# Performance work log

Hardware: AMD Instinct MI355X
Metric: run time of the kernel (lower is better)

The kernel has to match this reference:

```python
import jax, jax.numpy as jnp
import numpy as np
from jax import lax

B, N, CIN, COUT = 8, 4096, 64, 128
S, NS, V = 1024, 32, 4
RADIUS = 0.2
H1, H2 = 64, 128
BN_EPS = 1e-5


def _fps(xyz, n_sample):
    # farthest point sampling, deterministic start at index 0
    Bb, Nn, _ = xyz.shape
    start = jnp.zeros((Bb,), jnp.int32)
    mind0 = jnp.full((Bb, Nn), jnp.inf, xyz.dtype)

    def body(carry, _):
        mind, last = carry
        p = jnp.take_along_axis(xyz, last[:, None, None], axis=1)  # [B,1,3]
        d = jnp.sum((xyz - p) ** 2, -1)                             # [B,N]
        mind = jnp.minimum(mind, d)
        nxt = jnp.argmax(mind, -1).astype(jnp.int32)
        return (mind, nxt), nxt

    (_, _), rest = lax.scan(body, (mind0, start), None, length=n_sample - 1)
    idx = jnp.concatenate([start[None], rest], 0).T                 # [B,S]
    new_xyz = jnp.take_along_axis(xyz, idx[..., None], axis=1)      # [B,S,3]
    return new_xyz, idx


def _ball_query_idx(new_xyz, xyz, K, radius):
    # first K points (in index order) within radius, padded with -1
    d2 = jnp.sum((new_xyz[:, :, None, :] - xyz[:, None, :, :]) ** 2, -1)  # [B,S,N]
    within = d2 < radius * radius
    Nn = xyz.shape[1]
    ar = jnp.arange(Nn)
    key = jnp.where(within, ar, Nn + ar)            # in-ball points sort first, stably by index
    sel = jnp.argsort(key, axis=-1)[:, :, :K]       # [B,S,K]
    valid = jnp.take_along_axis(within, sel, axis=-1)
    return jnp.where(valid, sel, -1)


def _masked_gather(f, idx):
    # gather rows of f [B,N,C] with idx (any batched shape); idx==-1 -> zeros
    mask = idx == -1
    safe = jnp.where(mask, 0, idx)
    g = jax.vmap(lambda fb, ib: fb[ib])(f, safe)
    return jnp.where(mask[..., None], jnp.zeros((), f.dtype), g)


def _bn(x, gamma, beta, axes):
    # training-mode batchnorm over `axes` (channel is last dim)
    mu = jnp.mean(x, axes, keepdims=True)
    var = jnp.mean((x - mu) ** 2, axes, keepdims=True)
    return (x - mu) * (gamma / jnp.sqrt(var + BN_EPS)) + beta


def setup_inputs() -> dict:
    key = jax.random.key(0)
    ks = jax.random.split(key, 16)
    sc = 0.05
    inp = {
        "xyz": jax.random.uniform(ks[0], (B, N, 3), jnp.float32),
        "f": jax.random.normal(ks[1], (B, N, CIN), jnp.float32),
        "centroid_idx": jax.random.randint(ks[2], (V,), 0, NS),
        "affine_weight": jnp.ones((CIN + 6,), jnp.float32),
        "affine_bias": jnp.zeros((CIN + 6,), jnp.float32),
        "mix_w": sc * jax.random.normal(ks[3], (CIN, 2 * CIN + 6), jnp.float32),
        "mix_b": jnp.zeros((CIN,), jnp.float32),
        "m1_w1": sc * jax.random.normal(ks[4], (H1, 13), jnp.float32),
        "m1_b1": jnp.zeros((H1,), jnp.float32),
        "m1_g1": jnp.ones((H1,), jnp.float32),
        "m1_be1": jnp.zeros((H1,), jnp.float32),
        "m1_w2": sc * jax.random.normal(ks[5], (CIN, H1), jnp.float32),
        "m1_b2": jnp.zeros((CIN,), jnp.float32),
        "m2_w1": sc * jax.random.normal(ks[6], (H2, CIN), jnp.float32),
        "m2_b1": jnp.zeros((H2,), jnp.float32),
        "m2_g1": jnp.ones((H2,), jnp.float32),
        "m2_be1": jnp.zeros((H2,), jnp.float32),
        "m2_w2": sc * jax.random.normal(ks[7], (COUT, H2), jnp.float32),
        "m2_b2": jnp.zeros((COUT,), jnp.float32),
        "res_w": sc * jax.random.normal(ks[8], (COUT, CIN), jnp.float32),
        "res_b": jnp.zeros((COUT,), jnp.float32),
    }
    return inp


def reference(xyz, f, centroid_idx, affine_weight, affine_bias, mix_w, mix_b,
              m1_w1, m1_b1, m1_g1, m1_be1, m1_w2, m1_b2,
              m2_w1, m2_b1, m2_g1, m2_be1, m2_w2, m2_b2, res_w, res_b):
    Bb = xyz.shape[0]
    # ---- Grouping ----
    new_xyz, new_idx = _fps(xyz, S)                     # [B,S,3], [B,S]
    gidx = _ball_query_idx(new_xyz, xyz, NS, RADIUS)    # [B,S,n]
    mask = gidx == -1
    grouped_xyz = _masked_gather(xyz, gidx)             # [B,S,n,3]
    grouped_feat = _masked_gather(f, gidx)              # [B,S,n,cin]
    sampled = _masked_gather(f, new_idx)[:, :, None, :]  # [B,S,1,cin]
    gxl = grouped_xyz - new_xyz[:, :, None, :]
    gfl = grouped_feat - sampled
    gf = jnp.concatenate([grouped_xyz, gxl, gfl], -1)   # [B,S,n,cin+6]
    std = jnp.std(gf.reshape(Bb, -1), axis=-1, ddof=1).reshape(Bb, 1, 1, 1)
    gf = gf / (std + 1e-5)
    gf = affine_weight * gf + affine_bias
    gf = jnp.concatenate([gf, jnp.broadcast_to(sampled, (Bb, S, NS, CIN))], -1)
    grouped_f = jnp.einsum('bsnc,oc->bsno', gf, mix_w) + mix_b  # [B,S,n,cin]
    group_skip = grouped_f

    # ---- multi-centroid relative geometry (rel_jk, 13 channels) ----
    mc = xyz[:, centroid_idx, :]                                       # [B,V,3]
    arrow = grouped_xyz[:, :, :, None, :] - mc[:, None, None, :, :]    # [B,S,n,V,3]
    eu = jnp.sqrt(jnp.sum(arrow ** 2, -1, keepdims=True))              # [B,S,n,V,1]
    gx_b = jnp.broadcast_to(grouped_xyz[:, :, :, None, :], arrow.shape)
    mc_b = jnp.broadcast_to(mc[:, None, None, :, :], arrow.shape)
    rel = jnp.concatenate([-arrow, arrow, eu, gx_b, mc_b], -1)         # [B,S,n,V,13]

    # ---- m1: 1x1x1 Conv3d -> BN3d -> GELU -> Conv3d ----
    h = jnp.einsum('bsnvc,oc->bsnvo', rel, m1_w1) + m1_b1
    h = _bn(h, m1_g1, m1_be1, (0, 1, 2, 3))
    h = jax.nn.gelu(h, approximate=False)
    w_jk = jnp.einsum('bsnvc,oc->bsnvo', h, m1_w2) + m1_b2             # [B,S,n,V,cin]

    # ---- gumbel-softmax weighted aggregation over V centroids ----
    logits = grouped_f[:, :, :, None, :] * w_jk                        # [B,S,n,V,cin]
    u = jax.random.uniform(jax.random.key(42), logits.shape, logits.dtype, 1e-9, 1.0)
    gumbel = -jnp.log(-jnp.log(u))
    soft_w = jax.nn.softmax(logits + gumbel, axis=3)  # softmax over V (tau=1, soft)
    agg = jnp.sum(soft_w * logits, axis=3)                             # [B,S,n,cin]
    agg = agg + group_skip
    agg = jnp.where(mask[..., None], jnp.zeros((), agg.dtype), agg)

    # ---- m2: 1x1 Conv2d -> BN2d -> Conv2d, residual, max-pool over n ----
    h2 = jnp.einsum('bsnc,oc->bsno', agg, m2_w1) + m2_b1
    h2 = _bn(h2, m2_g1, m2_be1, (0, 1, 2))
    out = jnp.einsum('bsnc,oc->bsno', h2, m2_w2) + m2_b2               # [B,S,n,cout]
    res = jnp.einsum('bsnc,oc->bsno', group_skip, res_w) + res_b
    new_f = jax.nn.gelu(out + res, approximate=False)
    new_f = jnp.max(new_f, axis=2)                                     # [B,S,cout]
    return new_f, new_xyz
```

## Files before the change

kernel.cpp:

```cpp
#include <hip/hip_runtime.h>
#include <cstdint>
#include <cstddef>

#define TF_PARTITIONABLE 1

constexpr int B_ = 8, N_ = 4096, CIN_ = 64, COUT_ = 128;
constexpr int S_ = 1024, NS_ = 32, V_ = 4;
constexpr int ROWS_ = B_ * S_ * NS_;

constexpr size_t OFF_ACC   = 0;
constexpr size_t ACC_BYTES = 35072;
constexpr size_t OFF_SCALE = 35072;
constexpr size_t OFF_W1P   = 35328;
constexpr size_t OFF_B1P   = 38656;
constexpr size_t OFF_WCOMB = 38912;
constexpr size_t OFF_BCOMB = 71680;
constexpr size_t OFF_MIXWT = 72192;
constexpr size_t OFF_NIDX  = 106496;
constexpr size_t OFF_GIDX  = 139264;
constexpr size_t OFF_GF    = 1187840;
constexpr size_t OFF_AGG   = 68296704;

constexpr int AC_BATCH = 0;
constexpr int AC_G     = 16;
constexpr int AC_E     = 88;
constexpr int AC_S2A   = 216;
constexpr int AC_M2    = 280;

__device__ __forceinline__ float erf_fast(float x) {
    float ax = fabsf(x);
    float t = 1.0f / (1.0f + 0.3275911f * ax);
    float y = t * (0.254829592f + t * (-0.284496736f + t * (1.421413741f +
              t * (-1.453152027f + t * 1.061405429f))));
    float r = 1.0f - y * __expf(-ax * ax);
    return copysignf(r, x);
}

__device__ __forceinline__ float gelu_f(float x) {
    return 0.5f * x * (1.0f + erf_fast(x * 0.7071067811865476f));
}

#define TF_ROUND(r) { x0 += x1; x1 = (x1 << (r)) | (x1 >> (32 - (r))); x1 ^= x0; }

__device__ __forceinline__ unsigned tf_random_bits(unsigned lo) {
    const unsigned ks0 = 0u, ks1 = 42u, ks2 = 0x1BD11BDAu ^ 0u ^ 42u;
#if TF_PARTITIONABLE
    unsigned x0 = 0u + ks0, x1 = lo + ks1;
#else
    unsigned j = lo & 0x01FFFFFFu;
    unsigned x0 = j + ks0, x1 = (j + 0x02000000u) + ks1;
#endif
    TF_ROUND(13) TF_ROUND(15) TF_ROUND(26) TF_ROUND(6)
    x0 += ks1; x1 += ks2 + 1u;
    TF_ROUND(17) TF_ROUND(29) TF_ROUND(16) TF_ROUND(24)
    x0 += ks2; x1 += ks0 + 2u;
    TF_ROUND(13) TF_ROUND(15) TF_ROUND(26) TF_ROUND(6)
    x0 += ks0; x1 += ks1 + 3u;
    TF_ROUND(17) TF_ROUND(29) TF_ROUND(16) TF_ROUND(24)
    x0 += ks1; x1 += ks2 + 4u;
    TF_ROUND(13) TF_ROUND(15) TF_ROUND(26) TF_ROUND(6)
    x0 += ks2; x1 += ks0 + 5u;
#if TF_PARTITIONABLE
    return x0 ^ x1;
#else
    return (lo < 0x02000000u) ? x0 : x1;
#endif
}

__device__ __forceinline__ float gumbel_from_bits(unsigned bits) {
    float fl = __uint_as_float((bits >> 9) | 0x3f800000u) - 1.0f;
    float u  = fmaxf(1e-9f, fl + 1e-9f);
    float w = -logf(u);
    return -__logf(w);
}

__device__ __forceinline__ float wsum(float v) {
    for (int o = 32; o; o >>= 1) v += __shfl_down(v, o);
    return v;
}

__device__ __forceinline__ float wave_max64_nonneg(float v) {
    int x;
    x = __builtin_amdgcn_update_dpp(0, __float_as_int(v), 0xB1, 0xf, 0xf, true);
    v = fmaxf(v, __int_as_float(x));
    x = __builtin_amdgcn_update_dpp(0, __float_as_int(v), 0x4E, 0xf, 0xf, true);
    v = fmaxf(v, __int_as_float(x));
    x = __builtin_amdgcn_update_dpp(0, __float_as_int(v), 0x141, 0xf, 0xf, true);
    v = fmaxf(v, __int_as_float(x));
    x = __builtin_amdgcn_update_dpp(0, __float_as_int(v), 0x140, 0xf, 0xf, true);
    v = fmaxf(v, __int_as_float(x));
    x = __builtin_amdgcn_update_dpp(0, __float_as_int(v), 0x142, 0xf, 0xf, true);
    v = fmaxf(v, __int_as_float(x));
    x = __builtin_amdgcn_update_dpp(0, __float_as_int(v), 0x143, 0xf, 0xf, true);
    v = fmaxf(v, __int_as_float(x));
    return __int_as_float(__builtin_amdgcn_readlane(__float_as_int(v), 63));
}

__global__ __launch_bounds__(256) void k_fps(const float* __restrict__ xyz,
                                             int* __restrict__ new_idx,
                                             float* __restrict__ new_xyz) {
    __shared__ __align__(16) float4 sxyz[4096];
    __shared__ __align__(16) float swv[2][4];
    __shared__ __align__(16) int   swi[2][4];
    int b = blockIdx.x, t = threadIdx.x, lane = t & 63, wid = t >> 6;
    const float* xb = xyz + (size_t)b * 12288;
    float px[16], py[16], pz[16], md[16];
    int i0 = t * 16;
#pragma unroll
    for (int j = 0; j < 16; j++) {
        int i = i0 + j;
        float x = xb[i * 3], y = xb[i * 3 + 1], z = xb[i * 3 + 2];
        px[j] = x; py[j] = y; pz[j] = z;
        sxyz[i] = make_float4(x, y, z, 0.0f);
        md[j] = __builtin_inff();
    }
    __syncthreads();
    float4 c0 = sxyz[0];
    float cx = c0.x, cy = c0.y, cz = c0.z;
    if (t == 0) {
        new_idx[b * 1024] = 0;
        new_xyz[(size_t)b * 3072 + 0] = cx;
        new_xyz[(size_t)b * 3072 + 1] = cy;
        new_xyz[(size_t)b * 3072 + 2] = cz;
    }
    int p = 0;
    for (int it = 1; it < 1024; ++it) {
        float bv = -1.0f; int bj = 0;
#pragma unroll
        for (int j = 0; j < 16; j++) {
            float dx = __fsub_rn(px[j], cx), dy = __fsub_rn(py[j], cy), dz = __fsub_rn(pz[j], cz);
            float d = __fadd_rn(__fadd_rn(__fmul_rn(dx, dx), __fmul_rn(dy, dy)), __fmul_rn(dz, dz));
            float m2 = fminf(md[j], d); md[j] = m2;
            if (m2 > bv) { bv = m2; bj = j; }
        }
        float mx = wave_max64_nonneg(bv);
        unsigned long long msk = __ballot(bv == mx);
        int winlane = __ffsll(msk) - 1;
        if (lane == winlane) { swv[p][wid] = bv; swi[p][wid] = i0 + bj; }
        __syncthreads();
        float4 vv = *(const float4*)&swv[p][0];
        int4   ii4 = *(const int4*)&swi[p][0];
        float best = vv.x; int ii = ii4.x;
        if (vv.y > best) { best = vv.y; ii = ii4.y; }
        if (vv.z > best) { best = vv.z; ii = ii4.z; }
        if (vv.w > best) { best = vv.w; ii = ii4.w; }
        float4 cw = sxyz[ii];
        cx = cw.x; cy = cw.y; cz = cw.z;
        if (t == 0) {
            new_idx[b * 1024 + it] = ii;
            size_t o3 = ((size_t)b * 1024 + it) * 3;
            new_xyz[o3] = cx; new_xyz[o3 + 1] = cy; new_xyz[o3 + 2] = cz;
        }
        p ^= 1;
    }
}

__global__ __launch_bounds__(256) void k_ball(const float* __restrict__ xyz,
                                              const float* __restrict__ new_xyz,
                                              int* __restrict__ gidx) {
    int gw = blockIdx.x * 4 + (threadIdx.x >> 6);
    int lane = threadIdx.x & 63;
    int b = gw >> 10;
    const float* xb = xyz + (size_t)b * 12288;
    float qx = new_xyz[gw * 3], qy = new_xyz[gw * 3 + 1], qz = new_xyz[gw * 3 + 2];
    int* out = gidx + (size_t)gw * 32;
    int have = 0;
    for (int c0 = 0; c0 < 4096; c0 += 64) {
        int i = c0 + lane;
        float dx = __fsub_rn(qx, xb[i * 3]);
        float dy = __fsub_rn(qy, xb[i * 3 + 1]);
        float dz = __fsub_rn(qz, xb[i * 3 + 2]);
        float d2 = __fadd_rn(__fadd_rn(__fmul_rn(dx, dx), __fmul_rn(dy, dy)), __fmul_rn(dz, dz));
        bool within = d2 < 0.04f;
        unsigned long long mv = __ballot(within);
        int rank = __popcll(mv & ((1ull << lane) - 1ull));
        int pos = have + rank;
        if (within && pos < 32) out[pos] = i;
        have += (int)__popcll(mv);
        if (have >= 32) break;
    }
    for (int j = have + lane; j < 32; j += 64) out[j] = -1;
}

__global__ __launch_bounds__(256) void k_stats(const float* __restrict__ xyz,
                                               const float* __restrict__ f,
                                               const int* __restrict__ cidx,
                                               const int* __restrict__ new_idx,
                                               const int* __restrict__ gidx,
                                               const float* __restrict__ new_xyz,
                                               double* __restrict__ acc) {
    int b = blockIdx.x >> 5, blk = blockIdx.x & 31;
    int t = threadIdx.x, lane = t & 63;
    const float* xb = xyz + (size_t)b * 12288;
    const float* fb = f + ((size_t)b << 18);
    float mc[4][3];
#pragma unroll
    for (int v = 0; v < 4; v++) {
        int ci = cidx[v];
        mc[v][0] = xb[ci * 3]; mc[v][1] = xb[ci * 3 + 1]; mc[v][2] = xb[ci * 3 + 2];
    }
    float sum = 0.f, ssq = 0.f;
    float G1x = 0, G1y = 0, G1z = 0, Gxx = 0, Gxy = 0, Gxz = 0, Gyy = 0, Gyz = 0, Gzz = 0;
    float E1[4] = {0, 0, 0, 0}, Eax[4] = {0, 0, 0, 0}, Eay[4] = {0, 0, 0, 0}, Eaz[4] = {0, 0, 0, 0};
    for (int rr = 0; rr < 4; ++rr) {
        int row = blk * 1024 + rr * 256 + t;
        int s = row >> 5;
        int gi = gidx[((size_t)b << 15) + row];
        bool msk = gi < 0;
        int sg = (b << 10) + s;
        float nx = new_xyz[sg * 3], ny = new_xyz[sg * 3 + 1], nz = new_xyz[sg * 3 + 2];
        int nid = new_idx[sg];
        float gx = 0, gy = 0, gz = 0;
        if (!msk) { gx = xb[gi * 3]; gy = xb[gi * 3 + 1]; gz = xb[gi * 3 + 2]; }
        float a3 = __fsub_rn(gx, nx), a4 = __fsub_rn(gy, ny), a5 = __fsub_rn(gz, nz);
        sum += gx + gy + gz + a3 + a4 + a5;
        ssq += gx * gx + gy * gy + gz * gz + a3 * a3 + a4 * a4 + a5 * a5;
        const float4* fsp = (const float4*)(fb + ((size_t)nid << 6));
        int gi0 = msk ? 0 : gi;
        const float4* fip = (const float4*)(fb + ((size_t)gi0 << 6));
#pragma unroll
        for (int c4 = 0; c4 < 16; c4++) {
            float4 fs4 = fsp[c4];
            float4 fi4 = fip[c4];
            if (msk) { fi4.x = 0; fi4.y = 0; fi4.z = 0; fi4.w = 0; }
            float d0 = __fsub_rn(fi4.x, fs4.x), d1 = __fsub_rn(fi4.y, fs4.y);
            float d2 = __fsub_rn(fi4.z, fs4.z), d3 = __fsub_rn(fi4.w, fs4.w);
            sum += d0 + d1 + d2 + d3;
            ssq += d0 * d0 + d1 * d1 + d2 * d2 + d3 * d3;
        }
        G1x += gx; G1y += gy; G1z += gz;
        Gxx += gx * gx; Gxy += gx * gy; Gxz += gx * gz;
        Gyy += gy * gy; Gyz += gy * gz; Gzz += gz * gz;
#pragma unroll
        for (int v = 0; v < 4; v++) {
            float ax = __fsub_rn(gx, mc[v][0]), ay = __fsub_rn(gy, mc[v][1]), az = __fsub_rn(gz, mc[v][2]);
            float e = __fsqrt_rn(ax * ax + ay * ay + az * az);
            E1[v] += e; Eax[v] += e * gx; Eay[v] += e * gy; Eaz[v] += e * gz;
        }
    }
    sum = wsum(sum); ssq = wsum(ssq);
    G1x = wsum(G1x); G1y = wsum(G1y); G1z = wsum(G1z);
    Gxx = wsum(Gxx); Gxy = wsum(Gxy); Gxz = wsum(Gxz);
    Gyy = wsum(Gyy); Gyz = wsum(Gyz); Gzz = wsum(Gzz);
#pragma unroll
    for (int v = 0; v < 4; v++) {
        E1[v] = wsum(E1[v]); Eax[v] = wsum(Eax[v]); Eay[v] = wsum(Eay[v]); Eaz[v] = wsum(Eaz[v]);
    }
    if (lane == 0) {
        atomicAdd(&acc[AC_BATCH + b * 2 + 0], (double)sum);
        atomicAdd(&acc[AC_BATCH + b * 2 + 1], (double)ssq);
        double* Gb = acc + AC_G + b * 9;
        atomicAdd(&Gb[0], (double)G1x); atomicAdd(&Gb[1], (double)G1y); atomicAdd(&Gb[2], (double)G1z);
        atomicAdd(&Gb[3], (double)Gxx); atomicAdd(&Gb[4], (double)Gxy); atomicAdd(&Gb[5], (double)Gxz);
        atomicAdd(&Gb[6], (double)Gyy); atomicAdd(&Gb[7], (double)Gyz); atomicAdd(&Gb[8], (double)Gzz);
#pragma unroll
        for (int v = 0; v < 4; v++) {
            double* Eb = acc + AC_E + (b * 4 + v) * 4;
            atomicAdd(&Eb[0], (double)E1[v]);
            atomicAdd(&Eb[1], (double)Eax[v]);
            atomicAdd(&Eb[2], (double)Eay[v]);
            atomicAdd(&Eb[3], (double)Eaz[v]);
        }
    }
}

struct GS { double G1[3]; double G2[6]; double E1; double Ea[3]; double m[3]; };

__device__ __forceinline__ int g2i(int x, int y) {
    if (x > y) { int tt = x; x = y; y = tt; }
    return (x == 0) ? y : ((x == 1) ? (2 + y) : 5);
}

__device__ double pairsum(const GS& g, int ki, int ai, int kj, int aj) {
    const double R = 32768.0;
    if (ki > kj) { int tk = ki; ki = kj; kj = tk; int ta = ai; ai = aj; aj = ta; }
    switch (ki * 4 + kj) {
        case 0:  return g.G2[g2i(ai, aj)] - g.m[ai] * g.G1[aj] - g.m[aj] * g.G1[ai] + R * g.m[ai] * g.m[aj];
        case 1:  return g.Ea[ai] - g.m[ai] * g.E1;
        case 2:  return g.G2[g2i(ai, aj)] - g.m[ai] * g.G1[aj];
        case 3:  return (g.G1[ai] - R * g.m[ai]) * g.m[aj];
        case 5:  { double s = 0; for (int x = 0; x < 3; x++) s += g.G2[g2i(x, x)] - 2.0 * g.m[x] * g.G1[x] + R * g.m[x] * g.m[x]; return s; }
        case 6:  return g.Ea[aj];
        case 7:  return g.E1 * g.m[aj];
        case 10: return g.G2[g2i(ai, aj)];
        case 11: return g.G1[ai] * g.m[aj];
        case 15: return R * g.m[ai] * g.m[aj];
    }
    return 0.0;
}

__device__ __forceinline__ void chdec(int ch, int& kind, int& ax, double& sgn) {
    if (ch < 3)      { kind = 0; ax = ch;      sgn = -1.0; }
    else if (ch < 6) { kind = 0; ax = ch - 3;  sgn = 1.0; }
    else if (ch == 6){ kind = 1; ax = 0;       sgn = 1.0; }
    else if (ch < 10){ kind = 2; ax = ch - 7;  sgn = 1.0; }
    else             { kind = 3; ax = ch - 10; sgn = 1.0; }
}

__device__ GS load_gs(const double* acc, const float* xyz, const int* cidx, int grp) {
    GS g; int b = grp >> 2, v = grp & 3;
    const double* Gb = acc + AC_G + b * 9;
    g.G1[0] = Gb[0]; g.G1[1] = Gb[1]; g.G1[2] = Gb[2];
    for (int q = 0; q < 6; q++) g.G2[q] = Gb[3 + q];
    const double* Eb = acc + AC_E + grp * 4;
    g.E1 = Eb[0]; g.Ea[0] = Eb[1]; g.Ea[1] = Eb[2]; g.Ea[2] = Eb[3];
    int ci = cidx[v];
    g.m[0] = (double)xyz[(size_t)b * 12288 + ci * 3];
    g.m[1] = (double)xyz[(size_t)b * 12288 + ci * 3 + 1];
    g.m[2] = (double)xyz[(size_t)b * 12288 + ci * 3 + 2];
    return g;
}

__global__ __launch_bounds__(256) void k_prep(const double* __restrict__ acc,
                                              const float* __restrict__ xyz,
                                              const int* __restrict__ cidx,
                                              const float* __restrict__ m1w1,
                                              const float* __restrict__ m1b1,
                                              const float* __restrict__ m1g1,
                                              const float* __restrict__ m1be1,
                                              const float* __restrict__ mixw,
                                              float* __restrict__ scale,
                                              float* __restrict__ w1p,
                                              float* __restrict__ b1p,
                                              float* __restrict__ mixwt) {
    __shared__ double Sec[169];
    __shared__ double S1[13];
    int t = threadIdx.x;
    if (t < 8) {
        double sm = acc[AC_BATCH + t * 2], sq = acc[AC_BATCH + t * 2 + 1];
        double M = 2293760.0;
        double var = (sq - sm * sm / M) / (M - 1.0);
        float stdv = (float)sqrt(var);
        scale[t] = 1.0f / (stdv + 1e-5f);
    }
    for (int idx = t; idx < 8576; idx += 256) {
        int k = idx >> 6, o = idx & 63;
        mixwt[idx] = mixw[o * 134 + k];
    }
    if (t < 169) {
        int i = t / 13, j = t % 13;
        int ki, ai, kj, aj; double si, sj;
        chdec(i, ki, ai, si); chdec(j, kj, aj, sj);
        double val = 0;
        for (int grp = 0; grp < 32; grp++) {
            GS g = load_gs(acc, xyz, cidx, grp);
            val += si * sj * pairsum(g, ki, ai, kj, aj);
        }
        Sec[t] = val;
    } else if (t < 182) {
        int i = t - 169;
        int ki, ai; double si;
        chdec(i, ki, ai, si);
        double val = 0;
        const double R = 32768.0;
        for (int grp = 0; grp < 32; grp++) {
            GS g = load_gs(acc, xyz, cidx, grp);
            double tv;
            switch (ki) {
                case 0:  tv = si * (g.G1[ai] - R * g.m[ai]); break;
                case 1:  tv = g.E1; break;
                case 2:  tv = g.G1[ai]; break;
                default: tv = R * g.m[ai]; break;
            }
            val += tv;
        }
        S1[i] = val;
    }
    __syncthreads();
    if (t < 64) {
        double w[13];
        for (int k = 0; k < 13; k++) w[k] = (double)m1w1[t * 13 + k];
        double s1w = 0;
        for (int k = 0; k < 13; k++) s1w += w[k] * S1[k];
        double quad = 0;
        for (int i = 0; i < 13; i++) {
            double s = 0;
            for (int j = 0; j < 13; j++) s += Sec[i * 13 + j] * w[j];
            quad += w[i] * s;
        }
        double M1d = 1048576.0;
        double b1o = (double)m1b1[t];
        double mu = s1w / M1d + b1o;
        double E2 = (quad + 2.0 * b1o * s1w) / M1d + b1o * b1o;
        double var = E2 - mu * mu;
        double gg = (double)m1g1[t] / sqrt(var + 1e-5);
        for (int k = 0; k < 13; k++) w1p[t * 13 + k] = (float)(w[k] * gg);
        b1p[t] = (float)((b1o - mu) * gg + (double)m1be1[t]);
    }
}

__global__ __launch_bounds__(256) void k_groupedf(const float* __restrict__ xyz,
                                                  const float* __restrict__ f,
                                                  const int* __restrict__ new_idx,
                                                  const int* __restrict__ gidx,
                                                  const float* __restrict__ new_xyz,
                                                  const float* __restrict__ scale_p,
                                                  const float* __restrict__ aw,
                                                  const float* __restrict__ ab,
                                                  const float* __restrict__ mixwt,
                                                  const float* __restrict__ mixb,
                                                  float* __restrict__ gf) {
    int r = blockIdx.x * 256 + threadIdx.x;
    int b = r >> 15;
    int rb = r & 32767;
    int s = rb >> 5;
    int gi = gidx[r];
    bool msk = gi < 0;
    int gi0 = msk ? 0 : gi;
    int sg = (b << 10) + s;
    int nid = new_idx[sg];
    float scale = scale_p[b];
    float nx = new_xyz[sg * 3], ny = new_xyz[sg * 3 + 1], nz = new_xyz[sg * 3 + 2];
    const float* xb = xyz + (size_t)b * 12288;
    const float* fb = f + ((size_t)b << 18);
    float gx = 0, gy = 0, gz = 0;
    if (!msk) { gx = xb[gi * 3]; gy = xb[gi * 3 + 1]; gz = xb[gi * 3 + 2]; }
    float acc[64];
#pragma unroll
    for (int o = 0; o < 64; o++) acc[o] = mixb[o];
    float va[6];
    va[0] = gx; va[1] = gy; va[2] = gz;
    va[3] = __fsub_rn(gx, nx); va[4] = __fsub_rn(gy, ny); va[5] = __fsub_rn(gz, nz);
#pragma unroll
    for (int k = 0; k < 6; k++) {
        float g = aw[k] * (va[k] * scale) + ab[k];
        const float* wt = mixwt + k * 64;
#pragma unroll
        for (int o = 0; o < 64; o++) acc[o] += g * wt[o];
    }
    const float4* fip = (const float4*)(fb + ((size_t)gi0 << 6));
    const float4* fsp = (const float4*)(fb + ((size_t)nid << 6));
    for (int c4 = 0; c4 < 16; c4++) {
        float4 fi = fip[c4];
        if (msk) { fi.x = 0; fi.y = 0; fi.z = 0; fi.w = 0; }
        float4 fs4 = fsp[c4];
        float dv[4] = {__fsub_rn(fi.x, fs4.x), __fsub_rn(fi.y, fs4.y),
                       __fsub_rn(fi.z, fs4.z), __fsub_rn(fi.w, fs4.w)};
#pragma unroll
        for (int u = 0; u < 4; u++) {
            int k = 6 + c4 * 4 + u;
            float g = aw[k] * (dv[u] * scale) + ab[k];
            const float* wt = mixwt + k * 64;
#pragma unroll
            for (int o = 0; o < 64; o++) acc[o] += g * wt[o];
        }
    }
    for (int c4 = 0; c4 < 16; c4++) {
        float4 fs4 = fsp[c4];
        float sv[4] = {fs4.x, fs4.y, fs4.z, fs4.w};
#pragma unroll
        for (int u = 0; u < 4; u++) {
            int k = 70 + c4 * 4 + u;
            const float* wt = mixwt + k * 64;
#pragma unroll
            for (int o = 0; o < 64; o++) acc[o] += sv[u] * wt[o];
        }
    }
    float4* dst = (float4*)(gf + ((size_t)r << 6));
#pragma unroll
    for (int c4 = 0; c4 < 16; c4++)
        dst[c4] = make_float4(acc[c4 * 4], acc[c4 * 4 + 1], acc[c4 * 4 + 2], acc[c4 * 4 + 3]);
}

__global__ __launch_bounds__(256) void k_fused(const float* __restrict__ xyz,
                                               const int* __restrict__ cidx,
                                               const int* __restrict__ gidx,
                                               const float* __restrict__ gf,
                                               const float* __restrict__ w1p,
                                               const float* __restrict__ b1p,
                                               const float* __restrict__ w2,
                                               const float* __restrict__ b2,
                                               float* __restrict__ agg) {
    __shared__ float sh[4][4][64];
    __shared__ float smc[4][3];
    int t = threadIdx.x, wv = t >> 6, lane = t & 63;
    int row0 = blockIdx.x * 64;
    int b = row0 >> 15;
    if (t < 12) {
        int v = t / 3, j = t % 3;
        smc[v][j] = xyz[(size_t)b * 12288 + cidx[v] * 3 + j];
    }
    float w1l[13];
#pragma unroll
    for (int k = 0; k < 13; k++) w1l[k] = w1p[lane * 13 + k];
    float b1l = b1p[lane], b2l = b2[lane];
    float w2r[64];
#pragma unroll
    for (int c4 = 0; c4 < 16; c4++) {
        float4 tmp = *(const float4*)(w2 + lane * 64 + c4 * 4);
        w2r[c4 * 4] = tmp.x; w2r[c4 * 4 + 1] = tmp.y; w2r[c4 * 4 + 2] = tmp.z; w2r[c4 * 4 + 3] = tmp.w;
    }
    __syncthreads();
    float mcl[4][3];
#pragma unroll
    for (int v = 0; v < 4; v++) { mcl[v][0] = smc[v][0]; mcl[v][1] = smc[v][1]; mcl[v][2] = smc[v][2]; }
    int r = row0 + wv * 16;
    for (int rr = 0; rr < 16; ++rr, ++r) {
        int gi = gidx[r];
        bool msk = gi < 0;
        float gx = 0, gy = 0, gz = 0;
        if (!msk) {
            const float* p = xyz + (size_t)b * 12288 + (size_t)gi * 3;
            gx = p[0]; gy = p[1]; gz = p[2];
        }
        float gfo = gf[((size_t)r << 6) + lane];
#pragma unroll
        for (int v = 0; v < 4; v++) {
            float ax = __fsub_rn(gx, mcl[v][0]);
            float ay = __fsub_rn(gy, mcl[v][1]);
            float az = __fsub_rn(gz, mcl[v][2]);
            float eu = __fsqrt_rn(__fadd_rn(__fadd_rn(__fmul_rn(ax, ax), __fmul_rn(ay, ay)), __fmul_rn(az, az)));
            float h = b1l
                - ax * w1l[0] - ay * w1l[1] - az * w1l[2]
                + ax * w1l[3] + ay * w1l[4] + az * w1l[5]
                + eu * w1l[6] + gx * w1l[7] + gy * w1l[8] + gz * w1l[9]
                + mcl[v][0] * w1l[10] + mcl[v][1] * w1l[11] + mcl[v][2] * w1l[12];
            sh[wv][v][lane] = gelu_f(h);
        }
        float lg[4];
#pragma unroll
        for (int v = 0; v < 4; v++) {
            float a = b2l;
            const float4* hp = (const float4*)sh[wv][v];
#pragma unroll
            for (int c4 = 0; c4 < 16; c4++) {
                float4 hh = hp[c4];
                a += hh.x * w2r[c4 * 4] + hh.y * w2r[c4 * 4 + 1] + hh.z * w2r[c4 * 4 + 2] + hh.w * w2r[c4 * 4 + 3];
            }
            lg[v] = gfo * a;
        }
        unsigned base = ((unsigned)r << 8) + (unsigned)lane;
        float z0 = lg[0] + gumbel_from_bits(tf_random_bits(base));
        float z1 = lg[1] + gumbel_from_bits(tf_random_bits(base + 64u));
        float z2 = lg[2] + gumbel_from_bits(tf_random_bits(base + 128u));
        float z3 = lg[3] + gumbel_from_bits(tf_random_bits(base + 192u));
        float mx = fmaxf(fmaxf(z0, z1), fmaxf(z2, z3));
        float e0 = __expf(z0 - mx), e1 = __expf(z1 - mx), e2 = __expf(z2 - mx), e3 = __expf(z3 - mx);
        float inv = 1.0f / (e0 + e1 + e2 + e3);
        float av = (e0 * lg[0] + e1 * lg[1] + e2 * lg[2] + e3 * lg[3]) * inv + gfo;
        agg[((size_t)r << 6) + lane] = msk ? 0.0f : av;
    }
}

__global__ __launch_bounds__(256) void k_syrk(const float* __restrict__ agg,
                                              double* __restrict__ acc) {
    __shared__ float As[128][64];
    int t = threadIdx.x;
    int ti = t >> 4, tj = t & 15;
    float C[4][4] = {};
    float cs = 0.f;
    size_t base = (size_t)blockIdx.x * 1024 * 64;
    for (int tile = 0; tile < 8; ++tile) {
        const float4* src = (const float4*)(agg + base + (size_t)tile * 128 * 64);
#pragma unroll
        for (int i = 0; i < 8; i++) {
            int idx = t + i * 256;
            ((float4*)As)[idx] = src[idx];
        }
        __syncthreads();
        for (int rr = 0; rr < 128; ++rr) {
            float4 a = *(const float4*)&As[rr][ti * 4];
            float4 bb = *(const float4*)&As[rr][tj * 4];
            C[0][0] += a.x * bb.x; C[0][1] += a.x * bb.y; C[0][2] += a.x * bb.z; C[0][3] += a.x * bb.w;
            C[1][0] += a.y * bb.x; C[1][1] += a.y * bb.y; C[1][2] += a.y * bb.z; C[1][3] += a.y * bb.w;
            C[2][0] += a.z * bb.x; C[2][1] += a.z * bb.y; C[2][2] += a.z * bb.z; C[2][3] += a.z * bb.w;
            C[3][0] += a.w * bb.x; C[3][1] += a.w * bb.y; C[3][2] += a.w * bb.z; C[3][3] += a.w * bb.w;
            if (t < 64) cs += As[rr][t];
        }
        __syncthreads();
    }
    double* M2 = acc + AC_M2;
#pragma unroll
    for (int i = 0; i < 4; i++)
#pragma unroll
        for (int j = 0; j < 4; j++)
            atomicAdd(&M2[(ti * 4 + i) * 64 + (tj * 4 + j)], (double)C[i][j]);
    if (t < 64) atomicAdd(&acc[AC_S2A + t], (double)cs);
}

__global__ __launch_bounds__(256) void k_comb(const double* __restrict__ acc,
                                              const float* __restrict__ m2w1,
                                              const float* __restrict__ m2b1,
                                              const float* __restrict__ m2g1,
                                              const float* __restrict__ m2be1,
                                              const float* __restrict__ m2w2,
                                              const float* __restrict__ m2b2,
                                              float* __restrict__ wcomb,
                                              float* __restrict__ bcomb) {
    __shared__ float W1s[128 * 64];
    __shared__ float g2s[128], ofss[128];
    int t = threadIdx.x;
    const double* S2a = acc + AC_S2A;
    const double* M2 = acc + AC_M2;
    if (t < 128) {
        float wf[64];
        for (int c = 0; c < 64; c++) wf[c] = m2w1[t * 64 + c];
        double sw = 0;
        for (int c = 0; c < 64; c++) sw += (double)wf[c] * S2a[c];
        double quad = 0;
        for (int i = 0; i < 64; i++) {
            double s = 0;
            for (int j = 0; j < 64; j++) s += (double)wf[j] * M2[i * 64 + j];
            quad += (double)wf[i] * s;
        }
        double Rd = 262144.0;
        double b1o = (double)m2b1[t];
        double mu = sw / Rd + b1o;
        double E2 = (quad + 2.0 * b1o * sw) / Rd + b1o * b1o;
        double var = E2 - mu * mu;
        double gg = (double)m2g1[t] / sqrt(var + 1e-5);
        g2s[t] = (float)gg;
        ofss[t] = (float)(((double)m2b1[t] - mu) * gg + (double)m2be1[t]);
    }
    __syncthreads();
    for (int idx = t; idx < 128 * 64; idx += 256) {
        int c = idx >> 6, k = idx & 63;
        W1s[idx] = g2s[c] * m2w1[c * 64 + k];
    }
    __syncthreads();
    for (int idx = t; idx < 128 * 64; idx += 256) {
        int o = idx >> 6, k = idx & 63;
        float s = 0;
        for (int c = 0; c < 128; c++) s += m2w2[o * 128 + c] * W1s[c * 64 + k];
        wcomb[idx] = s;
    }
    if (t < 128) {
        float s = m2b2[t];
        for (int c = 0; c < 128; c++) s += m2w2[t * 128 + c] * ofss[c];
        bcomb[t] = s;
    }
}

__global__ __launch_bounds__(256) void k_final(const float* __restrict__ agg,
                                               const float* __restrict__ gf,
                                               const float* __restrict__ wcomb,
                                               const float* __restrict__ bcomb,
                                               const float* __restrict__ resw,
                                               const float* __restrict__ resb,
                                               float* __restrict__ out_f) {
    __shared__ float rbuf[8][128];
    int t = threadIdx.x, wv = t >> 6, lane = t & 63;
    int which = lane >> 5, n = lane & 31;
    int gw = blockIdx.x * 8 + wv * 2 + which;
    size_t r = (size_t)gw * 32 + n;
    float ar[64], sk[64];
    const float4* ap = (const float4*)(agg + (r << 6));
    const float4* sp = (const float4*)(gf + (r << 6));
#pragma unroll
    for (int c4 = 0; c4 < 16; c4++) {
        float4 x = ap[c4];
        ar[c4 * 4] = x.x; ar[c4 * 4 + 1] = x.y; ar[c4 * 4 + 2] = x.z; ar[c4 * 4 + 3] = x.w;
        float4 y = sp[c4];
        sk[c4 * 4] = y.x; sk[c4 * 4 + 1] = y.y; sk[c4 * 4 + 2] = y.z; sk[c4 * 4 + 3] = y.w;
    }
    for (int o = 0; o < 128; o++) {
        float a1 = bcomb[o], a2 = resb[o];
        const float* wc = wcomb + o * 64;
        const float* rw = resw + o * 64;
#pragma unroll
        for (int c = 0; c < 64; c++) { a1 += ar[c] * wc[c]; a2 += sk[c] * rw[c]; }
        float g = gelu_f(a1 + a2);
#pragma unroll
        for (int off = 16; off; off >>= 1) g = fmaxf(g, __shfl_xor(g, off));
        if (n == 0) rbuf[wv * 2 + which][o] = g;
    }
    __syncthreads();
    int base = blockIdx.x * 8;
    for (int i = t; i < 1024; i += 256) {
        int lr = i >> 7, o = i & 127;
        out_f[(size_t)(base + lr) * 128 + o] = rbuf[lr][o];
    }
}

extern "C" void kernel_launch(void* const* d_in, const int* in_sizes, int n_in,
                              void* d_out, int out_size, void* d_ws, size_t ws_size,
                              hipStream_t stream) {
    (void)in_sizes; (void)n_in; (void)out_size; (void)ws_size;
    const float* xyz  = (const float*)d_in[0];
    const float* f    = (const float*)d_in[1];
    const int*   cidx = (const int*)d_in[2];
    const float* aw   = (const float*)d_in[3];
    const float* ab   = (const float*)d_in[4];
    const float* mixw = (const float*)d_in[5];
    const float* mixb = (const float*)d_in[6];
    const float* m1w1 = (const float*)d_in[7];
    const float* m1b1 = (const float*)d_in[8];
    const float* m1g1 = (const float*)d_in[9];
    const float* m1be1= (const float*)d_in[10];
    const float* m1w2 = (const float*)d_in[11];
    const float* m1b2 = (const float*)d_in[12];
    const float* m2w1 = (const float*)d_in[13];
    const float* m2b1 = (const float*)d_in[14];
    const float* m2g1 = (const float*)d_in[15];
    const float* m2be1= (const float*)d_in[16];
    const float* m2w2 = (const float*)d_in[17];
    const float* m2b2 = (const float*)d_in[18];
    const float* resw = (const float*)d_in[19];
    const float* resb = (const float*)d_in[20];

    float* out_f   = (float*)d_out;
    float* out_xyz = out_f + (size_t)B_ * S_ * COUT_;

    char* ws = (char*)d_ws;
    double* acc  = (double*)(ws + OFF_ACC);
    float* scale = (float*)(ws + OFF_SCALE);
    float* w1p   = (float*)(ws + OFF_W1P);
    float* b1p   = (float*)(ws + OFF_B1P);
    float* wcomb = (float*)(ws + OFF_WCOMB);
    float* bcomb = (float*)(ws + OFF_BCOMB);
    float* mixwt = (float*)(ws + OFF_MIXWT);
    int*   nidx  = (int*)(ws + OFF_NIDX);
    int*   gidx  = (int*)(ws + OFF_GIDX);
    float* gf    = (float*)(ws + OFF_GF);
    float* agg   = (float*)(ws + OFF_AGG);

    hipMemsetAsync(ws, 0, ACC_BYTES, stream);
    hipLaunchKernelGGL(k_fps,      dim3(8),    dim3(256),  0, stream, xyz, nidx, out_xyz);
    hipLaunchKernelGGL(k_ball,     dim3(2048), dim3(256),  0, stream, xyz, out_xyz, gidx);
    hipLaunchKernelGGL(k_stats,    dim3(256),  dim3(256),  0, stream, xyz, f, cidx, nidx, gidx, out_xyz, acc);
    hipLaunchKernelGGL(k_prep,     dim3(1),    dim3(256),  0, stream, acc, xyz, cidx, m1w1, m1b1, m1g1, m1be1, mixw, scale, w1p, b1p, mixwt);
    hipLaunchKernelGGL(k_groupedf, dim3(1024), dim3(256),  0, stream, xyz, f, nidx, gidx, out_xyz, scale, aw, ab, mixwt, mixb, gf);
    hipLaunchKernelGGL(k_fused,    dim3(4096), dim3(256),  0, stream, xyz, cidx, gidx, gf, w1p, b1p, m1w2, m1b2, agg);
    hipLaunchKernelGGL(k_syrk,     dim3(256),  dim3(256),  0, stream, agg, acc);
    hipLaunchKernelGGL(k_comb,     dim3(1),    dim3(256),  0, stream, acc, m2w1, m2b1, m2g1, m2be1, m2w2, m2b2, wcomb, bcomb);
    hipLaunchKernelGGL(k_final,    dim3(1024), dim3(256),  0, stream, agg, gf, wcomb, bcomb, resw, resb, out_f);
}
```

Before: 2.000 ms.

## Carry winner coordinates through LDS in FPS, prefetch rows in fused kernel, fold memset

In the FPS kernel, each wave now writes its winning point's coordinates alongside its distance into shared memory. This removes the 64KB shared copy of all points and the dependent LDS lookup that sat on the serial critical path of each iteration. The fused kernel software-prefetches the next row's gather index, coordinates and features while computing the current row, and gets a launch-bounds occupancy hint. The accumulator memset is folded into block 0 of the FPS kernel, which saves one stream operation but adds a little work to that block.

```diff
diff --git a/kernel.cpp b/kernel.cpp
--- a/kernel.cpp
+++ b/kernel.cpp
@@ -96,27 +96,28 @@
     return __int_as_float(__builtin_amdgcn_readlane(__float_as_int(v), 63));
 }
 
-__global__ __launch_bounds__(256) void k_fps(const float* __restrict__ xyz,
-                                             int* __restrict__ new_idx,
-                                             float* __restrict__ new_xyz) {
-    __shared__ __align__(16) float4 sxyz[4096];
-    __shared__ __align__(16) float swv[2][4];
-    __shared__ __align__(16) int   swi[2][4];
+__global__ __launch_bounds__(256, 1) void k_fps(const float* __restrict__ xyz,
+                                                int* __restrict__ new_idx,
+                                                float* __restrict__ new_xyz,
+                                                float* __restrict__ acc_zero) {
+    __shared__ __align__(16) float4 swc[2][4];
+    __shared__ __align__(16) int    swi[2][4];
     int b = blockIdx.x, t = threadIdx.x, lane = t & 63, wid = t >> 6;
+    if (b == 0) {
+        float4* az = (float4*)acc_zero;
+        for (int i = t; i < (int)(ACC_BYTES / 16); i += 256)
+            az[i] = make_float4(0.f, 0.f, 0.f, 0.f);
+    }
     const float* xb = xyz + (size_t)b * 12288;
     float px[16], py[16], pz[16], md[16];
     int i0 = t * 16;
 #pragma unroll
     for (int j = 0; j < 16; j++) {
         int i = i0 + j;
-        float x = xb[i * 3], y = xb[i * 3 + 1], z = xb[i * 3 + 2];
-        px[j] = x; py[j] = y; pz[j] = z;
-        sxyz[i] = make_float4(x, y, z, 0.0f);
+        px[j] = xb[i * 3]; py[j] = xb[i * 3 + 1]; pz[j] = xb[i * 3 + 2];
         md[j] = __builtin_inff();
     }
-    __syncthreads();
-    float4 c0 = sxyz[0];
-    float cx = c0.x, cy = c0.y, cz = c0.z;
+    float cx = xb[0], cy = xb[1], cz = xb[2];
     if (t == 0) {
         new_idx[b * 1024] = 0;
         new_xyz[(size_t)b * 3072 + 0] = cx;
@@ -136,16 +137,18 @@
         float mx = wave_max64_nonneg(bv);
         unsigned long long msk = __ballot(bv == mx);
         int winlane = __ffsll(msk) - 1;
-        if (lane == winlane) { swv[p][wid] = bv; swi[p][wid] = i0 + bj; }
+        if (lane == winlane) {
+            swc[p][wid] = make_float4(px[bj], py[bj], pz[bj], bv);
+            swi[p][wid] = i0 + bj;
+        }
         __syncthreads();
-        float4 vv = *(const float4*)&swv[p][0];
-        int4   ii4 = *(const int4*)&swi[p][0];
-        float best = vv.x; int ii = ii4.x;
-        if (vv.y > best) { best = vv.y; ii = ii4.y; }
-        if (vv.z > best) { best = vv.z; ii = ii4.z; }
-        if (vv.w > best) { best = vv.w; ii = ii4.w; }
-        float4 cw = sxyz[ii];
-        cx = cw.x; cy = cw.y; cz = cw.z;
+        float4 c0 = swc[p][0], c1 = swc[p][1], c2 = swc[p][2], c3 = swc[p][3];
+        int4 ii4 = *(const int4*)&swi[p][0];
+        float best = c0.w; float4 bc = c0; int ii = ii4.x;
+        if (c1.w > best) { best = c1.w; bc = c1; ii = ii4.y; }
+        if (c2.w > best) { best = c2.w; bc = c2; ii = ii4.z; }
+        if (c3.w > best) { best = c3.w; bc = c3; ii = ii4.w; }
+        cx = bc.x; cy = bc.y; cz = bc.z;
         if (t == 0) {
             new_idx[b * 1024 + it] = ii;
             size_t o3 = ((size_t)b * 1024 + it) * 3;
@@ -462,15 +465,15 @@
         dst[c4] = make_float4(acc[c4 * 4], acc[c4 * 4 + 1], acc[c4 * 4 + 2], acc[c4 * 4 + 3]);
 }
 
-__global__ __launch_bounds__(256) void k_fused(const float* __restrict__ xyz,
-                                               const int* __restrict__ cidx,
-                                               const int* __restrict__ gidx,
-                                               const float* __restrict__ gf,
-                                               const float* __restrict__ w1p,
-                                               const float* __restrict__ b1p,
-                                               const float* __restrict__ w2,
-                                               const float* __restrict__ b2,
-                                               float* __restrict__ agg) {
+__global__ __launch_bounds__(256, 3) void k_fused(const float* __restrict__ xyz,
+                                                  const int* __restrict__ cidx,
+                                                  const int* __restrict__ gidx,
+                                                  const float* __restrict__ gf,
+                                                  const float* __restrict__ w1p,
+                                                  const float* __restrict__ b1p,
+                                                  const float* __restrict__ w2,
+                                                  const float* __restrict__ b2,
+                                                  float* __restrict__ agg) {
     __shared__ float sh[4][4][64];
     __shared__ float smc[4][3];
     int t = threadIdx.x, wv = t >> 6, lane = t & 63;
@@ -494,16 +497,30 @@
     float mcl[4][3];
 #pragma unroll
     for (int v = 0; v < 4; v++) { mcl[v][0] = smc[v][0]; mcl[v][1] = smc[v][1]; mcl[v][2] = smc[v][2]; }
+    const float* xzb = xyz + (size_t)b * 12288;
+
     int r = row0 + wv * 16;
-    for (int rr = 0; rr < 16; ++rr, ++r) {
-        int gi = gidx[r];
-        bool msk = gi < 0;
-        float gx = 0, gy = 0, gz = 0;
-        if (!msk) {
-            const float* p = xyz + (size_t)b * 12288 + (size_t)gi * 3;
-            gx = p[0]; gy = p[1]; gz = p[2];
-        }
-        float gfo = gf[((size_t)r << 6) + lane];
+    int gi_n = gidx[r];
+    float gfo_n = gf[((size_t)r << 6) + lane];
+    float gx_n = 0, gy_n = 0, gz_n = 0;
+    if (gi_n >= 0) {
+        const float* pp = xzb + (size_t)gi_n * 3;
+        gx_n = pp[0]; gy_n = pp[1]; gz_n = pp[2];
+    }
+    for (int rr = 0; rr < 16; ++rr) {
+        int cr = r;
+        bool msk = gi_n < 0;
+        float gx = gx_n, gy = gy_n, gz = gz_n, gfo = gfo_n;
+        if (rr < 15) {
+            ++r;
+            gi_n = gidx[r];
+            gfo_n = gf[((size_t)r << 6) + lane];
+            gx_n = 0; gy_n = 0; gz_n = 0;
+            if (gi_n >= 0) {
+                const float* pp = xzb + (size_t)gi_n * 3;
+                gx_n = pp[0]; gy_n = pp[1]; gz_n = pp[2];
+            }
+        }
 #pragma unroll
         for (int v = 0; v < 4; v++) {
             float ax = __fsub_rn(gx, mcl[v][0]);
@@ -529,7 +546,7 @@
             }
             lg[v] = gfo * a;
         }
-        unsigned base = ((unsigned)r << 8) + (unsigned)lane;
+        unsigned base = ((unsigned)cr << 8) + (unsigned)lane;
         float z0 = lg[0] + gumbel_from_bits(tf_random_bits(base));
         float z1 = lg[1] + gumbel_from_bits(tf_random_bits(base + 64u));
         float z2 = lg[2] + gumbel_from_bits(tf_random_bits(base + 128u));
@@ -538,7 +555,7 @@
         float e0 = __expf(z0 - mx), e1 = __expf(z1 - mx), e2 = __expf(z2 - mx), e3 = __expf(z3 - mx);
         float inv = 1.0f / (e0 + e1 + e2 + e3);
         float av = (e0 * lg[0] + e1 * lg[1] + e2 * lg[2] + e3 * lg[3]) * inv + gfo;
-        agg[((size_t)r << 6) + lane] = msk ? 0.0f : av;
+        agg[((size_t)cr << 6) + lane] = msk ? 0.0f : av;
     }
 }
 
@@ -714,8 +731,7 @@
     float* gf    = (float*)(ws + OFF_GF);
     float* agg   = (float*)(ws + OFF_AGG);
 
-    hipMemsetAsync(ws, 0, ACC_BYTES, stream);
-    hipLaunchKernelGGL(k_fps,      dim3(8),    dim3(256),  0, stream, xyz, nidx, out_xyz);
+    hipLaunchKernelGGL(k_fps,      dim3(8),    dim3(256),  0, stream, xyz, nidx, out_xyz, (float*)acc);
     hipLaunchKernelGGL(k_ball,     dim3(2048), dim3(256),  0, stream, xyz, out_xyz, gidx);
     hipLaunchKernelGGL(k_stats,    dim3(256),  dim3(256),  0, stream, xyz, f, cidx, nidx, gidx, out_xyz, acc);
     hipLaunchKernelGGL(k_prep,     dim3(1),    dim3(256),  0, stream, acc, xyz, cidx, m1w1, m1b1, m1g1, m1be1, mixw, scale, w1p, b1p, mixwt);
```

New measurement: 3.185 ms. +59.2%, slower.
